# Optimization experiments

Measured on AMD Instinct MI355X. Metric: run time of the kernel, lower is better.

## Reference

```python
import jax, jax.numpy as jnp
import numpy as np

NUM_HEADS = 16
MAX_FREQ = 10.0
LN_EPS = 1e-5
PI = float(np.pi)


def layer_norm(x, w, b):
    mu = jnp.mean(x, axis=-1, keepdims=True)
    var = jnp.mean(jnp.square(x - mu), axis=-1, keepdims=True)
    return (x - mu) * jax.lax.rsqrt(var + LN_EPS) * w + b


def rotate_half(x):
    # interleaved pairs: (x0,x1,x2,x3,...) -> (-x1,x0,-x3,x2,...)
    x1 = x[..., 0::2]
    x2 = x[..., 1::2]
    return jnp.stack((-x2, x1), axis=-1).reshape(x.shape)


def drofe(q, k, freqband, demo):
    # q, k: [B,H,N,D]; freqband: [N,2] (lower/upper band bound); demo: [B,2] (age, gender)
    D = q.shape[-1]
    freqs = jnp.linspace(1.0, MAX_FREQ / 2.0, D // 4).astype(q.dtype) * PI  # [D/4]
    ang = jnp.concatenate([freqband[:, 0:1] * freqs, freqband[:, 1:2] * freqs], axis=-1)  # [N, D/2]
    ang = jnp.repeat(ang, 2, axis=-1)  # [N, D]
    cos, sin = jnp.cos(ang), jnp.sin(ang)
    age = demo[:, 0][:, None, None, None]
    gender = demo[:, 1][:, None, None, None]
    q = q * cos * age + rotate_half(q) * sin * gender
    k = k * cos * age + rotate_half(k) * sin * gender
    return q, k


def setup_inputs() -> dict:
    key = jax.random.key(0)
    ks = jax.random.split(key, 16)
    B, N, C, F = 8, 1024, 1024, 4096
    s = 0.02
    return {
        "x": jax.random.normal(ks[0], (B, N, C), jnp.float32),
        "demographic_info": jax.random.uniform(ks[1], (B, 2), jnp.float32),
        "explanation": jax.random.normal(ks[2], (B, N, C), jnp.float32),
        "freqband": jax.random.uniform(ks[3], (N, 2), jnp.float32) * 50.0,
        "w_qkv": jax.random.normal(ks[4], (C, 3 * C), jnp.float32) * s,
        "w_proj": jax.random.normal(ks[5], (C, C), jnp.float32) * s,
        "b_proj": jnp.zeros((C,), jnp.float32),
        "gamma1": jnp.full((C,), 1e-5, jnp.float32),
        "gamma2": jnp.full((C,), 1e-5, jnp.float32),
        "ln1_w": jnp.ones((C,), jnp.float32),
        "ln1_b": jnp.zeros((C,), jnp.float32),
        "ln2_w": jnp.ones((C,), jnp.float32),
        "ln2_b": jnp.zeros((C,), jnp.float32),
        "w1": jax.random.normal(ks[6], (C, F), jnp.float32) * s,
        "b1": jnp.zeros((F,), jnp.float32),
        "w2": jax.random.normal(ks[7], (F, C), jnp.float32) * s,
        "b2": jnp.zeros((C,), jnp.float32),
    }


def reference(x, demographic_info, explanation, freqband, w_qkv, w_proj, b_proj,
              gamma1, gamma2, ln1_w, ln1_b, ln2_w, ln2_b, w1, b1, w2, b2):
    B, N, C = x.shape
    H = NUM_HEADS
    D = C // H

    def split_qkv(t):
        return (t @ w_qkv).reshape(B, N, 3, H, D).transpose(2, 0, 3, 1, 4)  # [3,B,H,N,D]

    v = split_qkv(x)[2]
    qkv_e = split_qkv(explanation)  # explanation-swap: q,k come from explanation
    q, k = qkv_e[0], qkv_e[1]
    q, k = drofe(q, k, freqband, demographic_info)

    attn = jax.nn.softmax(jnp.einsum('bhnd,bhmd->bhnm', q, k) * (D ** -0.5), axis=-1)
    o = jnp.einsum('bhnm,bhmd->bhnd', attn, v).transpose(0, 2, 1, 3).reshape(B, N, C)
    o = o @ w_proj + b_proj

    x = layer_norm(x + gamma1 * o, ln1_w, ln1_b)  # post-norm + LayerScale
    h = jax.nn.gelu(x @ w1 + b1, approximate=False) @ w2 + b2
    x = layer_norm(x + gamma2 * h, ln2_w, ln2_b)
    return x
```

## Files before the change

kernel.cpp:

```cpp
#include <hip/hip_runtime.h>
#include <hip/hip_bf16.h>
#include <math.h>

typedef __attribute__((ext_vector_type(8))) short bf16x8;
typedef __attribute__((ext_vector_type(8))) unsigned short u16x8;
typedef __attribute__((ext_vector_type(4))) float f32x4;
typedef __attribute__((ext_vector_type(4))) unsigned short u16x4;

__device__ inline unsigned short f2bf(float f) {
    union { float f; unsigned u; } v; v.f = f;
    unsigned r = (v.u + 0x7fff + ((v.u >> 16) & 1)) >> 16;
    return (unsigned short)r;
}
__device__ inline float bf2f(unsigned short u) {
    union { unsigned u; float f; } v; v.u = ((unsigned)u) << 16; return v.f;
}

#define GLL16(gp, lp) __builtin_amdgcn_global_load_lds(                      \
    (const __attribute__((address_space(1))) void*)(gp),                     \
    (__attribute__((address_space(3))) void*)(lp), 16, 0, 0)

template<int EPI, int OUT_BF>
__global__ __launch_bounds__(256, 4) void gemm2ph128(
    const unsigned short* __restrict__ A,
    const unsigned short* __restrict__ Bt,
    const float* __restrict__ bias,
    void* __restrict__ Cout,
    int M, int Nn, int K, int ldc)
{
    __shared__ unsigned char lds[2][16384];
    const int tid = threadIdx.x;
    const int w = tid >> 6, lane = tid & 63;
    const int lk = lane & 15, lg = lane >> 4;
    const int wr = w >> 1, wc = w & 1;
    const int nbn = Nn >> 7;
    const int nb = gridDim.x;
    int bid = blockIdx.x;
    int swz = (nb & 7) ? bid : (bid & 7) * (nb >> 3) + (bid >> 3);
    const int bm = (swz / nbn) << 7, bn = (swz % nbn) << 7;

    f32x4 acc[4][4] = {};

    auto stage = [&](int buf, int k0) {
        #pragma unroll
        for (int i = 0; i < 4; ++i) {
            int s = tid + i * 256;
            int r = s >> 2, c = s & 3;
            int cs = (c ^ r ^ (r >> 2)) & 3;
            const unsigned short* gp = (r < 128)
                ? A  + (size_t)(bm + r) * K + k0 + cs * 8
                : Bt + (size_t)(bn + (r - 128)) * K + k0 + cs * 8;
            GLL16(gp, &lds[buf][s * 16]);
        }
    };

    const int NT = K >> 5;
    stage(0, 0);
    __syncthreads();
    int cur = 0;
    for (int t = 0; t < NT; ++t) {
        if (t + 1 < NT) stage(cur ^ 1, (t + 1) << 5);
        bf16x8 af[4], bfr[4];
        #pragma unroll
        for (int m = 0; m < 4; ++m) {
            int row = wr * 64 + m * 16 + lk;
            int sl = (lg ^ row ^ (row >> 2)) & 3;
            af[m] = *(const bf16x8*)&lds[cur][row * 64 + sl * 16];
        }
        #pragma unroll
        for (int n = 0; n < 4; ++n) {
            int row = wc * 64 + n * 16 + lk;
            int sl = (lg ^ row ^ (row >> 2)) & 3;
            bfr[n] = *(const bf16x8*)&lds[cur][8192 + row * 64 + sl * 16];
        }
        #pragma unroll
        for (int m = 0; m < 4; ++m)
            #pragma unroll
            for (int n = 0; n < 4; ++n)
                acc[m][n] = __builtin_amdgcn_mfma_f32_16x16x32_bf16(af[m], bfr[n], acc[m][n], 0, 0, 0);
        __syncthreads();
        cur ^= 1;
    }

    #pragma unroll
    for (int m = 0; m < 4; ++m) {
        int row = bm + wr * 64 + m * 16 + lg * 4;
        #pragma unroll
        for (int n = 0; n < 4; ++n) {
            int col = bn + wc * 64 + n * 16 + lk;
            #pragma unroll
            for (int r = 0; r < 4; ++r) {
                float v = acc[m][n][r];
                if (EPI >= 1) v += bias[col];
                if (EPI == 2) {
                    float u = v * 0.7978845608f * (1.0f + 0.044715f * v * v);
                    v = v / (1.0f + __expf(-2.0f * u));
                }
                if (OUT_BF)
                    ((unsigned short*)Cout)[(size_t)(row + r) * ldc + col] = f2bf(v);
                else
                    ((float*)Cout)[(size_t)(row + r) * ldc + col] = v;
            }
        }
    }
}

__global__ __launch_bounds__(256) void cvt_bf16(
    const float* __restrict__ src, unsigned short* __restrict__ dst, int n)
{
    int i = (blockIdx.x * 256 + threadIdx.x) * 4;
    if (i < n) {
        float4 v = *(const float4*)(src + i);
        u16x4 o = { f2bf(v.x), f2bf(v.y), f2bf(v.z), f2bf(v.w) };
        *(u16x4*)(dst + i) = o;
    }
}

__global__ __launch_bounds__(256) void transpose_cvt(
    const float* __restrict__ src, unsigned short* __restrict__ dst, int R, int Cc)
{
    __shared__ float t[32][33];
    const int bc = blockIdx.x * 32, br = blockIdx.y * 32;
    const int tx = threadIdx.x & 31, ty = threadIdx.x >> 5;
    #pragma unroll
    for (int i = 0; i < 4; ++i)
        t[ty + i * 8][tx] = src[(size_t)(br + ty + i * 8) * Cc + bc + tx];
    __syncthreads();
    #pragma unroll
    for (int i = 0; i < 4; ++i)
        dst[(size_t)(bc + ty + i * 8) * R + br + tx] = f2bf(t[tx][ty + i * 8]);
}

__global__ __launch_bounds__(256) void drofe_bf(
    const unsigned short* __restrict__ QK, unsigned short* __restrict__ Qo,
    unsigned short* __restrict__ Ko,
    const float* __restrict__ freqband, const float* __restrict__ demo, int N)
{
    const float PI_F = 3.14159265358979323846f;
    int idx = blockIdx.x * 256 + threadIdx.x;
    int col2 = idx & 511;
    int row  = idx >> 9;
    int n = row & (N - 1), b = row >> 10;
    int i  = col2 & 31;
    int ii = (i < 16) ? i : i - 16;
    float fb = (i < 16) ? freqband[n * 2 + 0] : freqband[n * 2 + 1];
    float freq = (1.0f + (float)ii * (4.0f / 15.0f)) * PI_F;
    float ang = fb * freq;
    float cv = cosf(ang), sv = sinf(ang);
    float ca = cv * demo[b * 2 + 0];
    float sg = sv * demo[b * 2 + 1];
    const unsigned* qk = (const unsigned*)(QK + (size_t)row * 2048);
    unsigned qu = qk[col2], ku = qk[512 + col2];
    float qe = bf2f((unsigned short)qu), qo_ = bf2f((unsigned short)(qu >> 16));
    float ke = bf2f((unsigned short)ku), ko_ = bf2f((unsigned short)(ku >> 16));
    const float s8 = 0.125f;
    unsigned qres = (unsigned)f2bf((qe * ca - qo_ * sg) * s8)
                  | ((unsigned)f2bf((qo_ * ca + qe * sg) * s8) << 16);
    unsigned kres = (unsigned)f2bf(ke * ca - ko_ * sg)
                  | ((unsigned)f2bf(ko_ * ca + ke * sg) << 16);
    ((unsigned*)Qo)[(size_t)row * 512 + col2] = qres;
    ((unsigned*)Ko)[(size_t)row * 512 + col2] = kres;
}

__global__ __launch_bounds__(256) void attn_mfma(
    const unsigned short* __restrict__ Q, const unsigned short* __restrict__ K,
    const unsigned short* __restrict__ V, unsigned short* __restrict__ O,
    int B, int H, int N)
{
    __shared__ unsigned short Ks[64 * 64];
    __shared__ unsigned short Vt[64 * 72];
    __shared__ unsigned short Ps[4][16 * 72];

    const int bi = blockIdx.x;
    const int bh = (bi & 7) + 8 * ((bi >> 3) & 15);
    const int q0 = (bi >> 7) * 64;
    const int b = bh >> 4, h = bh & 15;
    const int tid = threadIdx.x;
    const int w = tid >> 6, lane = tid & 63;
    const int lg = lane >> 4, lk = lane & 15;

    bf16x8 qf[2];
    {
        const unsigned short* qrow = Q + (size_t)(b * N + q0 + w * 16 + lk) * 1024 + h * 64;
        qf[0] = *(const bf16x8*)(qrow + lg * 8);
        qf[1] = *(const bf16x8*)(qrow + 32 + lg * 8);
    }

    f32x4 o[4] = {};
    float m_run = -INFINITY, l_run = 0.f;

    for (int t0 = 0; t0 < N; t0 += 64) {
        const size_t kvbase = (size_t)(b * N + t0) * 1024 + h * 64;
        #pragma unroll
        for (int it = 0; it < 2; ++it) {
            int s = it * 256 + tid;
            int row = s >> 3, cb = (s & 7) << 4;
            int dby = cb ^ ((row & 7) << 4);
            GLL16(K + kvbase + (size_t)row * 1024 + (dby >> 1), &Ks[s * 8]);
        }
        {
            int c = tid >> 5, k0 = (tid & 31) * 2;
            const unsigned short* vp = V + kvbase + (size_t)k0 * 1024 + c * 8;
            u16x8 va = *(const u16x8*)vp;
            u16x8 vb = *(const u16x8*)(vp + 1024);
            #pragma unroll
            for (int j = 0; j < 8; ++j) {
                unsigned val = (unsigned)va[j] | ((unsigned)vb[j] << 16);
                *(unsigned*)&Vt[(c * 8 + j) * 72 + k0] = val;
            }
        }
        __syncthreads();

        f32x4 s4[4];
        __builtin_amdgcn_s_setprio(1);
        #pragma unroll
        for (int sub = 0; sub < 4; ++sub) {
            f32x4 acc = {0.f, 0.f, 0.f, 0.f};
            #pragma unroll
            for (int kh = 0; kh < 2; ++kh) {
                int cc = (kh * 64 + lg * 16) ^ ((lk & 7) << 4);
                bf16x8 kf = *(const bf16x8*)&Ks[(sub * 16 + lk) * 64 + (cc >> 1)];
                acc = __builtin_amdgcn_mfma_f32_16x16x32_bf16(kf, qf[kh], acc, 0, 0, 0);
            }
            s4[sub] = acc;
        }
        __builtin_amdgcn_s_setprio(0);

        float pmax = -INFINITY;
        #pragma unroll
        for (int sub = 0; sub < 4; ++sub)
            #pragma unroll
            for (int r = 0; r < 4; ++r) pmax = fmaxf(pmax, s4[sub][r]);
        pmax = fmaxf(pmax, __shfl_xor(pmax, 16));
        pmax = fmaxf(pmax, __shfl_xor(pmax, 32));

        if (!__all(pmax - m_run <= 8.0f)) {
            float mn = fmaxf(m_run, pmax);
            float corr = __expf(m_run - mn);
            m_run = mn;
            l_run *= corr;
            #pragma unroll
            for (int ds = 0; ds < 4; ++ds)
                #pragma unroll
                for (int r = 0; r < 4; ++r) o[ds][r] *= corr;
        }

        float psum = 0.f;
        unsigned pw[4][2];
        #pragma unroll
        for (int sub = 0; sub < 4; ++sub) {
            float p0 = __expf(s4[sub][0] - m_run);
            float p1 = __expf(s4[sub][1] - m_run);
            float p2 = __expf(s4[sub][2] - m_run);
            float p3 = __expf(s4[sub][3] - m_run);
            psum += (p0 + p1) + (p2 + p3);
            pw[sub][0] = (__float_as_uint(p0) >> 16) | (__float_as_uint(p1) & 0xffff0000u);
            pw[sub][1] = (__float_as_uint(p2) >> 16) | (__float_as_uint(p3) & 0xffff0000u);
        }
        psum += __shfl_xor(psum, 16);
        psum += __shfl_xor(psum, 32);
        l_run += psum;
        #pragma unroll
        for (int sub = 0; sub < 4; ++sub) {
            *(unsigned*)&Ps[w][lk * 72 + sub * 16 + lg * 4]     = pw[sub][0];
            *(unsigned*)&Ps[w][lk * 72 + sub * 16 + lg * 4 + 2] = pw[sub][1];
        }
        asm volatile("s_waitcnt lgkmcnt(0)" ::: "memory");

        __builtin_amdgcn_s_setprio(1);
        #pragma unroll
        for (int kh = 0; kh < 2; ++kh) {
            bf16x8 pf = *(const bf16x8*)&Ps[w][lk * 72 + kh * 32 + lg * 8];
            #pragma unroll
            for (int ds = 0; ds < 4; ++ds) {
                bf16x8 vf = *(const bf16x8*)&Vt[(ds * 16 + lk) * 72 + kh * 32 + lg * 8];
                o[ds] = __builtin_amdgcn_mfma_f32_16x16x32_bf16(vf, pf, o[ds], 0, 0, 0);
            }
        }
        __builtin_amdgcn_s_setprio(0);
        __syncthreads();
    }

    {
        unsigned short* orow = O + (size_t)(b * N + q0 + w * 16 + lk) * 1024 + h * 64;
        float rinv = 1.0f / l_run;
        #pragma unroll
        for (int ds = 0; ds < 4; ++ds) {
            u16x4 pk = { f2bf(o[ds][0] * rinv), f2bf(o[ds][1] * rinv),
                         f2bf(o[ds][2] * rinv), f2bf(o[ds][3] * rinv) };
            *(u16x4*)(orow + ds * 16 + lg * 4) = pk;
        }
    }
}

__global__ __launch_bounds__(256) void ln_res_kernel(
    const float* __restrict__ x, const unsigned short* __restrict__ y,
    const float* __restrict__ gamma, const float* __restrict__ w,
    const float* __restrict__ bia, float* __restrict__ out,
    unsigned short* __restrict__ out_bf, int C)
{
    const int row = blockIdx.x;
    __shared__ float buf[1024];
    __shared__ float red[8];
    const size_t base = (size_t)row * C;
    float s = 0.f, ss = 0.f;
    for (int c = threadIdx.x; c < C; c += 256) {
        float v = x[base + c] + gamma[c] * bf2f(y[base + c]);
        buf[c] = v; s += v; ss += v * v;
    }
    #pragma unroll
    for (int msk = 1; msk < 64; msk <<= 1) { s += __shfl_xor(s, msk); ss += __shfl_xor(ss, msk); }
    int wv = threadIdx.x >> 6, lane = threadIdx.x & 63;
    if (lane == 0) { red[wv * 2] = s; red[wv * 2 + 1] = ss; }
    __syncthreads();
    if (threadIdx.x == 0) {
        float S = 0.f, SS = 0.f;
        #pragma unroll
        for (int i = 0; i < 4; ++i) { S += red[2 * i]; SS += red[2 * i + 1]; }
        red[0] = S; red[1] = SS;
    }
    __syncthreads();
    float mu = red[0] / C;
    float var = red[1] / C - mu * mu;
    float rstd = rsqrtf(var + 1e-5f);
    for (int c = threadIdx.x; c < C; c += 256) {
        float v = (buf[c] - mu) * rstd * w[c] + bia[c];
        out[base + c] = v;
        if (out_bf) out_bf[base + c] = f2bf(v);
    }
}

extern "C" void kernel_launch(void* const* d_in, const int* in_sizes, int n_in,
                              void* d_out, int out_size, void* d_ws, size_t ws_size,
                              hipStream_t stream)
{
    const float* x      = (const float*)d_in[0];
    const float* demo   = (const float*)d_in[1];
    const float* expl   = (const float*)d_in[2];
    const float* fb     = (const float*)d_in[3];
    const float* w_qkv  = (const float*)d_in[4];
    const float* w_proj = (const float*)d_in[5];
    const float* b_proj = (const float*)d_in[6];
    const float* gamma1 = (const float*)d_in[7];
    const float* gamma2 = (const float*)d_in[8];
    const float* ln1_w  = (const float*)d_in[9];
    const float* ln1_b  = (const float*)d_in[10];
    const float* ln2_w  = (const float*)d_in[11];
    const float* ln2_b  = (const float*)d_in[12];
    const float* w1     = (const float*)d_in[13];
    const float* b1     = (const float*)d_in[14];
    const float* w2     = (const float*)d_in[15];
    const float* b2     = (const float*)d_in[16];
    float* out = (float*)d_out;

    const int B = 8, N = 1024, C = 1024, F = 4096, H = 16;
    const int M = B * N;
    const size_t Mi = 1048576;

    float* ws = (float*)d_ws;
    unsigned short* QKbf = (unsigned short*)ws;
    unsigned short* Obf  = (unsigned short*)ws;
    unsigned short* H2   = (unsigned short*)ws;
    unsigned short* Qbf  = (unsigned short*)(ws + 8 * Mi);
    unsigned short* Kbf  = (unsigned short*)(ws + 12 * Mi);
    unsigned short* Vbf  = (unsigned short*)(ws + 16 * Mi);
    unsigned short* Hid  = (unsigned short*)(ws + 8 * Mi);
    unsigned short* Ebf  = (unsigned short*)(ws + 24 * Mi);
    unsigned short* Xbf  = (unsigned short*)(ws + 28 * Mi);
    unsigned short* Pb   = (unsigned short*)(ws + 24 * Mi);
    float*          X1   = ws + 32 * Mi;
    unsigned short* X1bf = (unsigned short*)(ws + 40 * Mi);
    unsigned short* Wt   = (unsigned short*)(ws + 44 * Mi);
    unsigned short* wqkvT  = Wt;
    unsigned short* wprojT = Wt + (size_t)3145728;
    unsigned short* w1T    = wprojT + (size_t)1048576;
    unsigned short* w2T    = w1T + (size_t)4194304;

    dim3 blk(256);
    const int MC = M * C;

    hipLaunchKernelGGL(cvt_bf16, dim3(MC / 1024), blk, 0, stream, expl, Ebf, MC);
    hipLaunchKernelGGL(cvt_bf16, dim3(MC / 1024), blk, 0, stream, x, Xbf, MC);
    hipLaunchKernelGGL(transpose_cvt, dim3(96, 32), blk, 0, stream, w_qkv, wqkvT, C, 3 * C);
    hipLaunchKernelGGL(transpose_cvt, dim3(32, 32), blk, 0, stream, w_proj, wprojT, C, C);
    hipLaunchKernelGGL(transpose_cvt, dim3(128, 32), blk, 0, stream, w1, w1T, C, F);
    hipLaunchKernelGGL(transpose_cvt, dim3(32, 128), blk, 0, stream, w2, w2T, F, C);

    hipLaunchKernelGGL((gemm2ph128<0,1>), dim3(64 * 16), blk, 0, stream, Ebf, wqkvT, (const float*)nullptr, (void*)QKbf, M, 2048, C, 2048);
    hipLaunchKernelGGL((gemm2ph128<0,1>), dim3(64 * 8), blk, 0, stream, Xbf, wqkvT + (size_t)2048 * 1024, (const float*)nullptr, (void*)Vbf, M, 1024, C, 1024);

    hipLaunchKernelGGL(drofe_bf, dim3(M * 512 / 256), blk, 0, stream, QKbf, Qbf, Kbf, fb, demo, N);

    hipLaunchKernelGGL(attn_mfma, dim3(B * H * (N / 64)), blk, 0, stream, Qbf, Kbf, Vbf, Obf, B, H, N);

    hipLaunchKernelGGL((gemm2ph128<1,1>), dim3(64 * 8), blk, 0, stream, Obf, wprojT, b_proj, (void*)Pb, M, 1024, C, 1024);

    hipLaunchKernelGGL(ln_res_kernel, dim3(M), blk, 0, stream, x, Pb, gamma1, ln1_w, ln1_b, X1, X1bf, C);

    hipLaunchKernelGGL((gemm2ph128<2,1>), dim3(64 * 32), blk, 0, stream, X1bf, w1T, b1, (void*)Hid, M, F, C, F);
    hipLaunchKernelGGL((gemm2ph128<1,1>), dim3(64 * 8), blk, 0, stream, Hid, w2T, b2, (void*)H2, M, 1024, F, 1024);

    hipLaunchKernelGGL(ln_res_kernel, dim3(M), blk, 0, stream, X1, H2, gamma2, ln2_w, ln2_b, out, (unsigned short*)nullptr, C);
}
```

Before: 426.9 us.

## Fuse DRoPE into QK GEMM epilogue and process two query tiles per attention block

The QK projection GEMM gets a new epilogue that applies the rotary/demographic rotation in registers. It uses lane shuffles to fetch the paired element and writes scaled Q and K directly, so the standalone drofe kernel and its QK round trip through memory are gone. The attention kernel now handles 128 query rows per block as two 64-row tiles that share each staged K/V tile, halving K/V loads and the grid size at the cost of more registers. The epilogue uses fast __sincosf with possibly large angles, which may reduce accuracy, and the scattered bf16 stores may be uncoalesced.

```diff
diff --git a/kernel.cpp b/kernel.cpp
--- a/kernel.cpp
+++ b/kernel.cpp
@@ -26,6 +26,9 @@
     const unsigned short* __restrict__ Bt,
     const float* __restrict__ bias,
     void* __restrict__ Cout,
+    void* __restrict__ Cout2,
+    const float* __restrict__ fbq,
+    const float* __restrict__ demo,
     int M, int Nn, int K, int ldc)
 {
     __shared__ unsigned char lds[2][16384];
@@ -80,6 +83,41 @@
                 acc[m][n] = __builtin_amdgcn_mfma_f32_16x16x32_bf16(af[m], bfr[n], acc[m][n], 0, 0, 0);
         __syncthreads();
         cur ^= 1;
+    }
+
+    if (EPI == 3) {
+        const float PI_F = 3.14159265358979323846f;
+        const int b_ = bm >> 10;
+        const float age = demo[b_ * 2 + 0], gen = demo[b_ * 2 + 1];
+        #pragma unroll
+        for (int m = 0; m < 4; ++m) {
+            #pragma unroll
+            for (int n = 0; n < 4; ++n) {
+                int col = bn + wc * 64 + n * 16 + lk;
+                int i = (col & 63) >> 1;
+                int ii = (i < 16) ? i : i - 16;
+                float freq = (1.0f + (float)ii * (4.0f / 15.0f)) * PI_F;
+                int fsel = (i >= 16) ? 1 : 0;
+                #pragma unroll
+                for (int r = 0; r < 4; ++r) {
+                    int row = bm + wr * 64 + m * 16 + lg * 4 + r;
+                    float val = acc[m][n][r];
+                    float par = __shfl_xor(val, 1);
+                    int nn = row & 1023;
+                    float ang = fbq[nn * 2 + fsel] * freq;
+                    float sv, cv;
+                    __sincosf(ang, &sv, &cv);
+                    float ca = cv * age, sg = sv * gen;
+                    float res = (col & 1) ? (val * ca + par * sg)
+                                          : (val * ca - par * sg);
+                    if (col < 1024)
+                        ((unsigned short*)Cout)[(size_t)row * 1024 + col] = f2bf(res * 0.125f);
+                    else
+                        ((unsigned short*)Cout2)[(size_t)row * 1024 + col - 1024] = f2bf(res);
+                }
+            }
+        }
+        return;
     }
 
     #pragma unroll
@@ -131,38 +169,7 @@
         dst[(size_t)(bc + ty + i * 8) * R + br + tx] = f2bf(t[tx][ty + i * 8]);
 }
 
-__global__ __launch_bounds__(256) void drofe_bf(
-    const unsigned short* __restrict__ QK, unsigned short* __restrict__ Qo,
-    unsigned short* __restrict__ Ko,
-    const float* __restrict__ freqband, const float* __restrict__ demo, int N)
-{
-    const float PI_F = 3.14159265358979323846f;
-    int idx = blockIdx.x * 256 + threadIdx.x;
-    int col2 = idx & 511;
-    int row  = idx >> 9;
-    int n = row & (N - 1), b = row >> 10;
-    int i  = col2 & 31;
-    int ii = (i < 16) ? i : i - 16;
-    float fb = (i < 16) ? freqband[n * 2 + 0] : freqband[n * 2 + 1];
-    float freq = (1.0f + (float)ii * (4.0f / 15.0f)) * PI_F;
-    float ang = fb * freq;
-    float cv = cosf(ang), sv = sinf(ang);
-    float ca = cv * demo[b * 2 + 0];
-    float sg = sv * demo[b * 2 + 1];
-    const unsigned* qk = (const unsigned*)(QK + (size_t)row * 2048);
-    unsigned qu = qk[col2], ku = qk[512 + col2];
-    float qe = bf2f((unsigned short)qu), qo_ = bf2f((unsigned short)(qu >> 16));
-    float ke = bf2f((unsigned short)ku), ko_ = bf2f((unsigned short)(ku >> 16));
-    const float s8 = 0.125f;
-    unsigned qres = (unsigned)f2bf((qe * ca - qo_ * sg) * s8)
-                  | ((unsigned)f2bf((qo_ * ca + qe * sg) * s8) << 16);
-    unsigned kres = (unsigned)f2bf(ke * ca - ko_ * sg)
-                  | ((unsigned)f2bf(ko_ * ca + ke * sg) << 16);
-    ((unsigned*)Qo)[(size_t)row * 512 + col2] = qres;
-    ((unsigned*)Ko)[(size_t)row * 512 + col2] = kres;
-}
-
-__global__ __launch_bounds__(256) void attn_mfma(
+__global__ __launch_bounds__(256, 4) void attn_mfma(
     const unsigned short* __restrict__ Q, const unsigned short* __restrict__ K,
     const unsigned short* __restrict__ V, unsigned short* __restrict__ O,
     int B, int H, int N)
@@ -173,21 +180,23 @@
 
     const int bi = blockIdx.x;
     const int bh = (bi & 7) + 8 * ((bi >> 3) & 15);
-    const int q0 = (bi >> 7) * 64;
+    const int q0 = (bi >> 7) * 128;
     const int b = bh >> 4, h = bh & 15;
     const int tid = threadIdx.x;
     const int w = tid >> 6, lane = tid & 63;
     const int lg = lane >> 4, lk = lane & 15;
 
-    bf16x8 qf[2];
-    {
-        const unsigned short* qrow = Q + (size_t)(b * N + q0 + w * 16 + lk) * 1024 + h * 64;
-        qf[0] = *(const bf16x8*)(qrow + lg * 8);
-        qf[1] = *(const bf16x8*)(qrow + 32 + lg * 8);
-    }
-
-    f32x4 o[4] = {};
-    float m_run = -INFINITY, l_run = 0.f;
+    bf16x8 qf[2][2];
+    #pragma unroll
+    for (int qt = 0; qt < 2; ++qt) {
+        const unsigned short* qrow =
+            Q + (size_t)(b * N + q0 + qt * 64 + w * 16 + lk) * 1024 + h * 64;
+        qf[qt][0] = *(const bf16x8*)(qrow + lg * 8);
+        qf[qt][1] = *(const bf16x8*)(qrow + 32 + lg * 8);
+    }
+
+    f32x4 o[2][4] = {};
+    float m_run[2] = { -INFINITY, -INFINITY }, l_run[2] = { 0.f, 0.f };
 
     for (int t0 = 0; t0 < N; t0 += 64) {
         const size_t kvbase = (size_t)(b * N + t0) * 1024 + h * 64;
@@ -211,83 +220,88 @@
         }
         __syncthreads();
 
-        f32x4 s4[4];
-        __builtin_amdgcn_s_setprio(1);
-        #pragma unroll
-        for (int sub = 0; sub < 4; ++sub) {
-            f32x4 acc = {0.f, 0.f, 0.f, 0.f};
+        #pragma unroll
+        for (int qt = 0; qt < 2; ++qt) {
+            f32x4 s4[4];
+            __builtin_amdgcn_s_setprio(1);
+            #pragma unroll
+            for (int sub = 0; sub < 4; ++sub) {
+                f32x4 acc = {0.f, 0.f, 0.f, 0.f};
+                #pragma unroll
+                for (int kh = 0; kh < 2; ++kh) {
+                    int cc = (kh * 64 + lg * 16) ^ ((lk & 7) << 4);
+                    bf16x8 kf = *(const bf16x8*)&Ks[(sub * 16 + lk) * 64 + (cc >> 1)];
+                    acc = __builtin_amdgcn_mfma_f32_16x16x32_bf16(kf, qf[qt][kh], acc, 0, 0, 0);
+                }
+                s4[sub] = acc;
+            }
+            __builtin_amdgcn_s_setprio(0);
+
+            float pmax = -INFINITY;
+            #pragma unroll
+            for (int sub = 0; sub < 4; ++sub)
+                #pragma unroll
+                for (int r = 0; r < 4; ++r) pmax = fmaxf(pmax, s4[sub][r]);
+            pmax = fmaxf(pmax, __shfl_xor(pmax, 16));
+            pmax = fmaxf(pmax, __shfl_xor(pmax, 32));
+
+            if (!__all(pmax - m_run[qt] <= 8.0f)) {
+                float mn = fmaxf(m_run[qt], pmax);
+                float corr = __expf(m_run[qt] - mn);
+                m_run[qt] = mn;
+                l_run[qt] *= corr;
+                #pragma unroll
+                for (int ds = 0; ds < 4; ++ds)
+                    #pragma unroll
+                    for (int r = 0; r < 4; ++r) o[qt][ds][r] *= corr;
+            }
+
+            float psum = 0.f;
+            unsigned pw[4][2];
+            #pragma unroll
+            for (int sub = 0; sub < 4; ++sub) {
+                float p0 = __expf(s4[sub][0] - m_run[qt]);
+                float p1 = __expf(s4[sub][1] - m_run[qt]);
+                float p2 = __expf(s4[sub][2] - m_run[qt]);
+                float p3 = __expf(s4[sub][3] - m_run[qt]);
+                psum += (p0 + p1) + (p2 + p3);
+                pw[sub][0] = (__float_as_uint(p0) >> 16) | (__float_as_uint(p1) & 0xffff0000u);
+                pw[sub][1] = (__float_as_uint(p2) >> 16) | (__float_as_uint(p3) & 0xffff0000u);
+            }
+            psum += __shfl_xor(psum, 16);
+            psum += __shfl_xor(psum, 32);
+            l_run[qt] += psum;
+            #pragma unroll
+            for (int sub = 0; sub < 4; ++sub) {
+                *(unsigned*)&Ps[w][lk * 72 + sub * 16 + lg * 4]     = pw[sub][0];
+                *(unsigned*)&Ps[w][lk * 72 + sub * 16 + lg * 4 + 2] = pw[sub][1];
+            }
+            asm volatile("s_waitcnt lgkmcnt(0)" ::: "memory");
+
+            __builtin_amdgcn_s_setprio(1);
             #pragma unroll
             for (int kh = 0; kh < 2; ++kh) {
-                int cc = (kh * 64 + lg * 16) ^ ((lk & 7) << 4);
-                bf16x8 kf = *(const bf16x8*)&Ks[(sub * 16 + lk) * 64 + (cc >> 1)];
-                acc = __builtin_amdgcn_mfma_f32_16x16x32_bf16(kf, qf[kh], acc, 0, 0, 0);
-            }
-            s4[sub] = acc;
-        }
-        __builtin_amdgcn_s_setprio(0);
-
-        float pmax = -INFINITY;
-        #pragma unroll
-        for (int sub = 0; sub < 4; ++sub)
-            #pragma unroll
-            for (int r = 0; r < 4; ++r) pmax = fmaxf(pmax, s4[sub][r]);
-        pmax = fmaxf(pmax, __shfl_xor(pmax, 16));
-        pmax = fmaxf(pmax, __shfl_xor(pmax, 32));
-
-        if (!__all(pmax - m_run <= 8.0f)) {
-            float mn = fmaxf(m_run, pmax);
-            float corr = __expf(m_run - mn);
-            m_run = mn;
-            l_run *= corr;
-            #pragma unroll
-            for (int ds = 0; ds < 4; ++ds)
+                bf16x8 pf = *(const bf16x8*)&Ps[w][lk * 72 + kh * 32 + lg * 8];
                 #pragma unroll
-                for (int r = 0; r < 4; ++r) o[ds][r] *= corr;
-        }
-
-        float psum = 0.f;
-        unsigned pw[4][2];
-        #pragma unroll
-        for (int sub = 0; sub < 4; ++sub) {
-            float p0 = __expf(s4[sub][0] - m_run);
-            float p1 = __expf(s4[sub][1] - m_run);
-            float p2 = __expf(s4[sub][2] - m_run);
-            float p3 = __expf(s4[sub][3] - m_run);
-            psum += (p0 + p1) + (p2 + p3);
-            pw[sub][0] = (__float_as_uint(p0) >> 16) | (__float_as_uint(p1) & 0xffff0000u);
-            pw[sub][1] = (__float_as_uint(p2) >> 16) | (__float_as_uint(p3) & 0xffff0000u);
-        }
-        psum += __shfl_xor(psum, 16);
-        psum += __shfl_xor(psum, 32);
-        l_run += psum;
-        #pragma unroll
-        for (int sub = 0; sub < 4; ++sub) {
-            *(unsigned*)&Ps[w][lk * 72 + sub * 16 + lg * 4]     = pw[sub][0];
-            *(unsigned*)&Ps[w][lk * 72 + sub * 16 + lg * 4 + 2] = pw[sub][1];
-        }
-        asm volatile("s_waitcnt lgkmcnt(0)" ::: "memory");
-
-        __builtin_amdgcn_s_setprio(1);
-        #pragma unroll
-        for (int kh = 0; kh < 2; ++kh) {
-            bf16x8 pf = *(const bf16x8*)&Ps[w][lk * 72 + kh * 32 + lg * 8];
-            #pragma unroll
-            for (int ds = 0; ds < 4; ++ds) {
-                bf16x8 vf = *(const bf16x8*)&Vt[(ds * 16 + lk) * 72 + kh * 32 + lg * 8];
-                o[ds] = __builtin_amdgcn_mfma_f32_16x16x32_bf16(vf, pf, o[ds], 0, 0, 0);
-            }
-        }
-        __builtin_amdgcn_s_setprio(0);
+                for (int ds = 0; ds < 4; ++ds) {
+                    bf16x8 vf = *(const bf16x8*)&Vt[(ds * 16 + lk) * 72 + kh * 32 + lg * 8];
+                    o[qt][ds] = __builtin_amdgcn_mfma_f32_16x16x32_bf16(vf, pf, o[qt][ds], 0, 0, 0);
+                }
+            }
+            __builtin_amdgcn_s_setprio(0);
+        }
         __syncthreads();
     }
 
-    {
-        unsigned short* orow = O + (size_t)(b * N + q0 + w * 16 + lk) * 1024 + h * 64;
-        float rinv = 1.0f / l_run;
+    #pragma unroll
+    for (int qt = 0; qt < 2; ++qt) {
+        unsigned short* orow =
+            O + (size_t)(b * N + q0 + qt * 64 + w * 16 + lk) * 1024 + h * 64;
+        float rinv = 1.0f / l_run[qt];
         #pragma unroll
         for (int ds = 0; ds < 4; ++ds) {
-            u16x4 pk = { f2bf(o[ds][0] * rinv), f2bf(o[ds][1] * rinv),
-                         f2bf(o[ds][2] * rinv), f2bf(o[ds][3] * rinv) };
+            u16x4 pk = { f2bf(o[qt][ds][0] * rinv), f2bf(o[qt][ds][1] * rinv),
+                         f2bf(o[qt][ds][2] * rinv), f2bf(o[qt][ds][3] * rinv) };
             *(u16x4*)(orow + ds * 16 + lg * 4) = pk;
         }
     }
@@ -358,7 +372,6 @@
     const size_t Mi = 1048576;
 
     float* ws = (float*)d_ws;
-    unsigned short* QKbf = (unsigned short*)ws;
     unsigned short* Obf  = (unsigned short*)ws;
     unsigned short* H2   = (unsigned short*)ws;
     unsigned short* Qbf  = (unsigned short*)(ws + 8 * Mi);
@@ -386,19 +399,23 @@
     hipLaunchKernelGGL(transpose_cvt, dim3(128, 32), blk, 0, stream, w1, w1T, C, F);
     hipLaunchKernelGGL(transpose_cvt, dim3(32, 128), blk, 0, stream, w2, w2T, F, C);
 
-    hipLaunchKernelGGL((gemm2ph128<0,1>), dim3(64 * 16), blk, 0, stream, Ebf, wqkvT, (const float*)nullptr, (void*)QKbf, M, 2048, C, 2048);
-    hipLaunchKernelGGL((gemm2ph128<0,1>), dim3(64 * 8), blk, 0, stream, Xbf, wqkvT + (size_t)2048 * 1024, (const float*)nullptr, (void*)Vbf, M, 1024, C, 1024);
-
-    hipLaunchKernelGGL(drofe_bf, dim3(M * 512 / 256), blk, 0, stream, QKbf, Qbf, Kbf, fb, demo, N);
-
-    hipLaunchKernelGGL(attn_mfma, dim3(B * H * (N / 64)), blk, 0, stream, Qbf, Kbf, Vbf, Obf, B, H, N);
-
-    hipLaunchKernelGGL((gemm2ph128<1,1>), dim3(64 * 8), blk, 0, stream, Obf, wprojT, b_proj, (void*)Pb, M, 1024, C, 1024);
+    hipLaunchKernelGGL((gemm2ph128<3,1>), dim3(64 * 16), blk, 0, stream, Ebf, wqkvT,
+                       (const float*)nullptr, (void*)Qbf, (void*)Kbf, fb, demo, M, 2048, C, 2048);
+    hipLaunchKernelGGL((gemm2ph128<0,1>), dim3(64 * 8), blk, 0, stream, Xbf,
+                       wqkvT + (size_t)2048 * 1024, (const float*)nullptr, (void*)Vbf,
+                       (void*)nullptr, (const float*)nullptr, (const float*)nullptr, M, 1024, C, 1024);
+
+    hipLaunchKernelGGL(attn_mfma, dim3(B * H * (N / 128)), blk, 0, stream, Qbf, Kbf, Vbf, Obf, B, H, N);
+
+    hipLaunchKernelGGL((gemm2ph128<1,1>), dim3(64 * 8), blk, 0, stream, Obf, wprojT, b_proj,
+                       (void*)Pb, (void*)nullptr, (const float*)nullptr, (const float*)nullptr, M, 1024, C, 1024);
 
     hipLaunchKernelGGL(ln_res_kernel, dim3(M), blk, 0, stream, x, Pb, gamma1, ln1_w, ln1_b, X1, X1bf, C);
 
-    hipLaunchKernelGGL((gemm2ph128<2,1>), dim3(64 * 32), blk, 0, stream, X1bf, w1T, b1, (void*)Hid, M, F, C, F);
-    hipLaunchKernelGGL((gemm2ph128<1,1>), dim3(64 * 8), blk, 0, stream, Hid, w2T, b2, (void*)H2, M, 1024, F, 1024);
+    hipLaunchKernelGGL((gemm2ph128<2,1>), dim3(64 * 32), blk, 0, stream, X1bf, w1T, b1,
+                       (void*)Hid, (void*)nullptr, (const float*)nullptr, (const float*)nullptr, M, F, C, F);
+    hipLaunchKernelGGL((gemm2ph128<1,1>), dim3(64 * 8), blk, 0, stream, Hid, w2T, b2,
+                       (void*)H2, (void*)nullptr, (const float*)nullptr, (const float*)nullptr, M, 1024, F, 1024);
 
     hipLaunchKernelGGL(ln_res_kernel, dim3(M), blk, 0, stream, X1, H2, gamma2, ln2_w, ln2_b, out, (unsigned short*)nullptr, C);
 }
```

Measured after the change: 409.0 us. 4.2% less time.
